# Kernel tuning notes

Measured on AMD Instinct MI355X. Metric: run time of the kernel, lower is better.

## Reference

```python
import math
import jax, jax.numpy as jnp
import numpy as np

B, W, C = 2, 2048, 1024
N, K = 16, 64  # heads, head dim (C // N)


def setup_inputs() -> dict:
    key = jax.random.key(0)
    ks = jax.random.split(key, 6)
    return {
        "in_sequence_bwc": jax.random.normal(ks[0], (B, W, C), dtype=jnp.float32),
        "W_proj": jax.random.normal(ks[1], (C, C), dtype=jnp.float32) * (1.0 / math.sqrt(C)),
        "b_proj": jax.random.normal(ks[2], (C,), dtype=jnp.float32) * 0.01,
        "generators_1nwk": jax.random.normal(ks[3], (1, N, W, K), dtype=jnp.float32),
        "W_mix": jax.random.normal(ks[4], (C, C), dtype=jnp.float32) * (1.0 / math.sqrt(C)),
        "b_mix": jax.random.normal(ks[5], (C,), dtype=jnp.float32) * 0.01,
    }


def reference(in_sequence_bwc, W_proj, b_proj, generators_1nwk, W_mix, b_mix):
    b, w, c = in_sequence_bwc.shape
    # shared projection (torch Linear: x @ W.T + b)
    p_bwc = in_sequence_bwc @ W_proj.T + b_proj
    p_bnwk = p_bwc.reshape(b, w, N, K).transpose(0, 2, 1, 3)  # [b, n, w, k]
    g_nwk = generators_1nwk[0, :, :w, :]  # [n, w, k]
    # data-dependent metric generator: p^T @ G -> [b, n, k, k]
    m_bnkk = jnp.einsum("bnwk,nwl->bnkl", p_bnwk, g_nwk)
    tril_kk = jnp.tril(jnp.ones((K, K), dtype=in_sequence_bwc.dtype))
    m_bnkk = m_bnkk * tril_kk  # lower-triangular mask on k x k
    m_bnkk = m_bnkk @ jnp.swapaxes(m_bnkk, -1, -2)  # PSD metric M M^T
    # bilinear scores: P @ M @ P^T, scaled
    pm_bnwk = jnp.einsum("bnwk,bnkl->bnwl", p_bnwk, m_bnkk)
    scores_bnww = jnp.einsum("bnwk,bnvk->bnwv", pm_bnwk, p_bnwk) / math.sqrt(K)
    causal = jnp.tril(jnp.ones((w, w), dtype=bool))
    scores_bnww = jnp.where(causal, scores_bnww, -jnp.inf)
    attn_bnww = jax.nn.softmax(scores_bnww, axis=-1)
    nudged_bnwk = attn_bnww @ p_bnwk
    nudged_bwc = nudged_bnwk.transpose(0, 2, 1, 3).reshape(b, w, c)
    return nudged_bwc @ W_mix.T + b_mix
```

## Files before the change

### kernel.cpp

```cpp
#include <hip/hip_runtime.h>
#include <math.h>

#define B_  2
#define W_  2048
#define C_  1024
#define NH_ 16
#define KD_ 64

__device__ __forceinline__ int sw(int r, int c) {
    return (r << 6) + ((((c >> 2) ^ ((r >> 2) & 7)) << 2) | (c & 3));
}

__device__ __forceinline__ void stage64s(const float* __restrict__ src,
                                         float* dst, int tid) {
#pragma unroll
    for (int q = 0; q < 4; ++q) {
        int idx = tid + (q << 8);
        int r   = idx >> 4;
        int c   = (idx & 15) << 2;
        *(float4*)&dst[sw(r, c)] = *(const float4*)(src + (idx << 2));
    }
}

__device__ __forceinline__ void stage64(const float* __restrict__ src,
                                        float (*dst)[68], int tid) {
#pragma unroll
    for (int q = 0; q < 4; ++q) {
        int idx = tid + (q << 8);
        int e   = idx << 2;
        int r   = e >> 6;
        int c   = e & 63;
        *(float4*)&dst[r][c] = *(const float4*)(src + e);
    }
}

template<int OUT_P_LAYOUT>
__global__ __launch_bounds__(256, 2)
void gemm_nt(const float* __restrict__ A, const float* __restrict__ Bw,
             const float* __restrict__ bias, float* __restrict__ Cout)
{
    __shared__ float As[16][68];
    __shared__ float Bs[16][68];
    const int tid = threadIdx.x;
    const int tx  = tid & 15, ty = tid >> 4;
    const int m0  = blockIdx.x << 6;
    const int n0  = blockIdx.y << 6;
    const int lrow = tid >> 2;
    const int lkq  = (tid & 3) << 2;
    const float* Ap = A  + (size_t)(m0 + lrow) * C_ + lkq;
    const float* Bp = Bw + (size_t)(n0 + lrow) * C_ + lkq;

    float acc[4][4] = {};
    for (int k0 = 0; k0 < C_; k0 += 16) {
        float4 av = *(const float4*)(Ap + k0);
        float4 bv = *(const float4*)(Bp + k0);
        __syncthreads();
        As[lkq+0][lrow] = av.x; As[lkq+1][lrow] = av.y;
        As[lkq+2][lrow] = av.z; As[lkq+3][lrow] = av.w;
        Bs[lkq+0][lrow] = bv.x; Bs[lkq+1][lrow] = bv.y;
        Bs[lkq+2][lrow] = bv.z; Bs[lkq+3][lrow] = bv.w;
        __syncthreads();
#pragma unroll
        for (int kk = 0; kk < 16; ++kk) {
            float4 a4 = *(const float4*)&As[kk][ty << 2];
            float4 b4 = *(const float4*)&Bs[kk][tx << 2];
            float am[4] = {a4.x, a4.y, a4.z, a4.w};
            float bm[4] = {b4.x, b4.y, b4.z, b4.w};
#pragma unroll
            for (int i = 0; i < 4; ++i)
#pragma unroll
                for (int j = 0; j < 4; ++j)
                    acc[i][j] = fmaf(am[i], bm[j], acc[i][j]);
        }
    }

    const int gc = n0 + (tx << 2);
    float4 bb = *(const float4*)&bias[gc];
#pragma unroll
    for (int i = 0; i < 4; ++i) {
        int gm = m0 + (ty << 2) + i;
        float4 o;
        o.x = acc[i][0] + bb.x;
        o.y = acc[i][1] + bb.y;
        o.z = acc[i][2] + bb.z;
        o.w = acc[i][3] + bb.w;
        if (OUT_P_LAYOUT) {
            int b = gm >> 11;
            int w = gm & 2047;
            int n = gc >> 6;
            int k = gc & 63;
            *(float4*)(Cout + (((size_t)(b * NH_ + n) * W_ + w) * KD_ + k)) = o;
        } else {
            *(float4*)(Cout + (size_t)gm * C_ + gc) = o;
        }
    }
}

__global__ __launch_bounds__(256, 2)
void metric_part(const float* __restrict__ p, const float* __restrict__ g,
                 float* __restrict__ part)
{
    __shared__ float Ps[32][68];
    __shared__ float Gs[32][68];
    const int ch  = blockIdx.x;
    const int bn  = blockIdx.y;
    const int n   = bn & (NH_ - 1);
    const int tid = threadIdx.x;
    const int tx  = tid & 15, ty = tid >> 4;
    const float* pb = p + (size_t)bn * W_ * KD_ + (size_t)(ch << 8) * KD_;
    const float* gb = g + (size_t)n  * W_ * KD_ + (size_t)(ch << 8) * KD_;

    float acc[4][4] = {};
    for (int w0 = 0; w0 < 256; w0 += 32) {
        __syncthreads();
#pragma unroll
        for (int q = 0; q < 2; ++q) {
            int idx = tid + (q << 8);
            int e   = idx << 2;
            int r   = e >> 6;
            int c   = e & 63;
            *(float4*)&Ps[r][c] = *(const float4*)(pb + (size_t)(w0 + r) * KD_ + c);
            *(float4*)&Gs[r][c] = *(const float4*)(gb + (size_t)(w0 + r) * KD_ + c);
        }
        __syncthreads();
#pragma unroll 8
        for (int w = 0; w < 32; ++w) {
            float4 a4 = *(const float4*)&Ps[w][ty << 2];
            float4 b4 = *(const float4*)&Gs[w][tx << 2];
            float am[4] = {a4.x, a4.y, a4.z, a4.w};
            float bm[4] = {b4.x, b4.y, b4.z, b4.w};
#pragma unroll
            for (int i = 0; i < 4; ++i)
#pragma unroll
                for (int j = 0; j < 4; ++j)
                    acc[i][j] = fmaf(am[i], bm[j], acc[i][j]);
        }
    }

    float* ob = part + (size_t)(bn * 8 + ch) * KD_ * KD_;
#pragma unroll
    for (int i = 0; i < 4; ++i) {
        float4 o; o.x = acc[i][0]; o.y = acc[i][1]; o.z = acc[i][2]; o.w = acc[i][3];
        *(float4*)(ob + ((ty << 2) + i) * KD_ + (tx << 2)) = o;
    }
}

__global__ __launch_bounds__(256, 2)
void metric_reduce(const float* __restrict__ part, float* __restrict__ m2)
{
    __shared__ float M1s[64][68];
    const int bn  = blockIdx.x;
    const int tid = threadIdx.x;
    const int tx  = tid & 15, ty = tid >> 4;
    const float* pb = part + (size_t)bn * 8 * KD_ * KD_;

#pragma unroll
    for (int v = 0; v < 4; ++v) {
        int f = tid + (v << 8);
        int e = f << 2;
        float4 s = *(const float4*)(pb + e);
#pragma unroll
        for (int c = 1; c < 8; ++c) {
            float4 t = *(const float4*)(pb + c * 4096 + e);
            s.x += t.x; s.y += t.y; s.z += t.z; s.w += t.w;
        }
        int k = e >> 6, l = e & 63;
        if (l + 0 > k) s.x = 0.f;
        if (l + 1 > k) s.y = 0.f;
        if (l + 2 > k) s.z = 0.f;
        if (l + 3 > k) s.w = 0.f;
        *(float4*)&M1s[k][l] = s;
    }
    __syncthreads();

    float a2[4][4] = {};
#pragma unroll
    for (int jq = 0; jq < 64; jq += 4) {
        float4 av[4], bv[4];
#pragma unroll
        for (int i = 0; i < 4; ++i) av[i] = *(const float4*)&M1s[(ty << 2) + i][jq];
#pragma unroll
        for (int j = 0; j < 4; ++j) bv[j] = *(const float4*)&M1s[(tx << 2) + j][jq];
#pragma unroll
        for (int i = 0; i < 4; ++i)
#pragma unroll
            for (int j = 0; j < 4; ++j)
                a2[i][j] += av[i].x * bv[j].x + av[i].y * bv[j].y +
                            av[i].z * bv[j].z + av[i].w * bv[j].w;
    }

    float* ob = m2 + (size_t)bn * KD_ * KD_;
#pragma unroll
    for (int i = 0; i < 4; ++i) {
        float4 o; o.x = a2[i][0]; o.y = a2[i][1]; o.z = a2[i][2]; o.w = a2[i][3];
        *(float4*)(ob + ((ty << 2) + i) * KD_ + (tx << 2)) = o;
    }
}

__global__ __launch_bounds__(256, 2)
void qgen_k(const float* __restrict__ p, const float* __restrict__ m2,
            float* __restrict__ qout)
{
    __shared__ float Pt[64][68];
    __shared__ float Ms[64][68];
    const int bn  = blockIdx.y;
    const int w0  = blockIdx.x << 6;
    const int tid = threadIdx.x;
    const int tx  = tid & 15, ty = tid >> 4;
    const float* pb = p  + (size_t)bn * W_ * KD_ + (size_t)w0 * KD_;
    const float* mb = m2 + (size_t)bn * KD_ * KD_;

    stage64(pb, Pt, tid);
    stage64(mb, Ms, tid);
    __syncthreads();

    float acc[4][4] = {};
#pragma unroll
    for (int kq = 0; kq < 64; kq += 4) {
        float4 av[4];
        float  bm[4][4];
#pragma unroll
        for (int i = 0; i < 4; ++i) av[i] = *(const float4*)&Pt[(ty << 2) + i][kq];
#pragma unroll
        for (int kk = 0; kk < 4; ++kk) {
            float4 t = *(const float4*)&Ms[kq + kk][tx << 2];
            bm[kk][0] = t.x; bm[kk][1] = t.y; bm[kk][2] = t.z; bm[kk][3] = t.w;
        }
#pragma unroll
        for (int i = 0; i < 4; ++i) {
            float am[4] = {av[i].x, av[i].y, av[i].z, av[i].w};
#pragma unroll
            for (int j = 0; j < 4; ++j)
                acc[i][j] = fmaf(am[0], bm[0][j],
                            fmaf(am[1], bm[1][j],
                            fmaf(am[2], bm[2][j],
                            fmaf(am[3], bm[3][j], acc[i][j]))));
        }
    }

    float* ob = qout + (size_t)bn * W_ * KD_ + (size_t)w0 * KD_;
#pragma unroll
    for (int i = 0; i < 4; ++i) {
        float4 o;
        o.x = acc[i][0] * 0.125f; o.y = acc[i][1] * 0.125f;
        o.z = acc[i][2] * 0.125f; o.w = acc[i][3] * 0.125f;
        *(float4*)(ob + ((ty << 2) + i) * KD_ + (tx << 2)) = o;
    }
}

__global__ __launch_bounds__(256, 2)
void attn_k(const float* __restrict__ qg, const float* __restrict__ p,
            float* __restrict__ nud)
{
    __shared__ float Qs[4096];
    __shared__ float Ks[2][4096];
    __shared__ float Es[4096];
    const int bid = blockIdx.x;
    const int bn  = bid & 31;
    const int qt  = (bid < 512) ? (31 - (bid >> 5)) : ((bid - 512) >> 5);
    const int b   = bn >> 4, n = bn & 15;
    const int tid = threadIdx.x;
    const int tx  = tid & 15, ty = tid >> 4;
    const float* qb = qg + (size_t)bn * W_ * KD_ + (size_t)(qt << 6) * KD_;
    const float* kb = p  + (size_t)bn * W_ * KD_;

    stage64s(qb, Qs, tid);
    stage64s(kb, Ks[0], tid);
    __syncthreads();

    float acc[4][4] = {};
    float mi[4], li[4];
#pragma unroll
    for (int i = 0; i < 4; ++i) { mi[i] = -INFINITY; li[i] = 0.f; }

    float4 ld[4];

    for (int j0 = 0; j0 <= qt; ++j0) {
        const int cur = j0 & 1;
        float* Kc = Ks[cur];

        if (j0 < qt) {
            const float* nx = kb + (size_t)((j0 + 1) << 6) * KD_;
#pragma unroll
            for (int q = 0; q < 4; ++q)
                ld[q] = *(const float4*)(nx + ((tid + (q << 8)) << 2));
        }

        float s[4][4] = {};
#pragma unroll
        for (int kq = 0; kq < 16; ++kq) {
            float4 av[4], bv[4];
#pragma unroll
            for (int i = 0; i < 4; ++i)
                av[i] = *(const float4*)&Qs[sw((ty << 2) + i, kq << 2)];
#pragma unroll
            for (int j = 0; j < 4; ++j)
                bv[j] = *(const float4*)&Kc[sw((tx << 2) + j, kq << 2)];
#pragma unroll
            for (int i = 0; i < 4; ++i)
#pragma unroll
                for (int j = 0; j < 4; ++j)
                    s[i][j] = fmaf(av[i].x, bv[j].x,
                              fmaf(av[i].y, bv[j].y,
                              fmaf(av[i].z, bv[j].z,
                              fmaf(av[i].w, bv[j].w, s[i][j]))));
        }

        if (j0 == qt) {
#pragma unroll
            for (int i = 0; i < 4; ++i)
#pragma unroll
                for (int j = 0; j < 4; ++j)
                    if (((tx << 2) + j) > ((ty << 2) + i)) s[i][j] = -INFINITY;
        }

        float mnew[4], al[4];
#pragma unroll
        for (int i = 0; i < 4; ++i) {
            float rm = fmaxf(fmaxf(s[i][0], s[i][1]), fmaxf(s[i][2], s[i][3]));
            rm = fmaxf(rm, __shfl_xor(rm, 1, 16));
            rm = fmaxf(rm, __shfl_xor(rm, 2, 16));
            rm = fmaxf(rm, __shfl_xor(rm, 4, 16));
            rm = fmaxf(rm, __shfl_xor(rm, 8, 16));
            mnew[i] = fmaxf(mi[i], rm);
        }
#pragma unroll
        for (int i = 0; i < 4; ++i) {
#pragma unroll
            for (int j = 0; j < 4; ++j) s[i][j] = __expf(s[i][j] - mnew[i]);
            float rs = s[i][0] + s[i][1] + s[i][2] + s[i][3];
            rs += __shfl_xor(rs, 1, 16);
            rs += __shfl_xor(rs, 2, 16);
            rs += __shfl_xor(rs, 4, 16);
            rs += __shfl_xor(rs, 8, 16);
            al[i] = __expf(mi[i] - mnew[i]);
            li[i] = li[i] * al[i] + rs;
            mi[i] = mnew[i];
        }

        __syncthreads();

#pragma unroll
        for (int i = 0; i < 4; ++i) {
            float4 e; e.x = s[i][0]; e.y = s[i][1]; e.z = s[i][2]; e.w = s[i][3];
            *(float4*)&Es[sw((ty << 2) + i, tx << 2)] = e;
#pragma unroll
            for (int j = 0; j < 4; ++j) acc[i][j] *= al[i];
        }
        if (j0 < qt) {
            float* Kn = Ks[cur ^ 1];
#pragma unroll
            for (int q = 0; q < 4; ++q) {
                int idx = tid + (q << 8);
                *(float4*)&Kn[sw(idx >> 4, (idx & 15) << 2)] = ld[q];
            }
        }
        __syncthreads();

#pragma unroll
        for (int jq = 0; jq < 64; jq += 4) {
            float4 av[4];
            float  vm[4][4];
#pragma unroll
            for (int i = 0; i < 4; ++i) av[i] = *(const float4*)&Es[sw((ty << 2) + i, jq)];
#pragma unroll
            for (int kk = 0; kk < 4; ++kk) {
                float4 t = *(const float4*)&Kc[sw(jq + kk, tx << 2)];
                vm[kk][0] = t.x; vm[kk][1] = t.y; vm[kk][2] = t.z; vm[kk][3] = t.w;
            }
#pragma unroll
            for (int i = 0; i < 4; ++i) {
                float am[4] = {av[i].x, av[i].y, av[i].z, av[i].w};
#pragma unroll
                for (int c = 0; c < 4; ++c)
                    acc[i][c] = fmaf(am[0], vm[0][c],
                                fmaf(am[1], vm[1][c],
                                fmaf(am[2], vm[2][c],
                                fmaf(am[3], vm[3][c], acc[i][c]))));
            }
        }
    }

    const int wrow = qt << 6;
#pragma unroll
    for (int i = 0; i < 4; ++i) {
        float inv = 1.f / li[i];
        float4 o;
        o.x = acc[i][0] * inv; o.y = acc[i][1] * inv;
        o.z = acc[i][2] * inv; o.w = acc[i][3] * inv;
        size_t row = (size_t)(b * W_ + wrow + (ty << 2) + i);
        *(float4*)(nud + row * C_ + (n << 6) + (tx << 2)) = o;
    }
}

extern "C" void kernel_launch(void* const* d_in, const int* in_sizes, int n_in,
                              void* d_out, int out_size, void* d_ws, size_t ws_size,
                              hipStream_t stream)
{
    (void)in_sizes; (void)n_in; (void)out_size; (void)ws_size;
    const float* X  = (const float*)d_in[0];
    const float* Wp = (const float*)d_in[1];
    const float* bp = (const float*)d_in[2];
    const float* G  = (const float*)d_in[3];
    const float* Wm = (const float*)d_in[4];
    const float* bm = (const float*)d_in[5];
    float* out = (float*)d_out;
    float* ws  = (float*)d_ws;

    float* Pbuf = ws;
    float* Qbuf = ws + 4194304;
    float* M2   = ws + 8388608;
    float* Nud  = ws + 8519680;
    float* Part = Qbuf;

    dim3 blk(256);
    gemm_nt<1>   <<<dim3(64, 16), blk, 0, stream>>>(X, Wp, bp, Pbuf);
    metric_part  <<<dim3(8, 32),  blk, 0, stream>>>(Pbuf, G, Part);
    metric_reduce<<<dim3(32),     blk, 0, stream>>>(Part, M2);
    qgen_k       <<<dim3(32, 32), blk, 0, stream>>>(Pbuf, M2, Qbuf);
    attn_k       <<<dim3(1024),   blk, 0, stream>>>(Qbuf, Pbuf, Nud);
    gemm_nt<0>   <<<dim3(64, 16), blk, 0, stream>>>(Nud, Wm, bm, out);
}
```

Baseline: 802.6 us.

## Software-pipeline attention loop: compute next QK^T while doing current PV

Restructures the flash-attention loop so that the scores and softmax for key tile p0+1 are computed in the same iteration as the P·V accumulation for tile p0. The probability tile is double-buffered and the loop keeps a single barrier per iteration instead of two. Q and V (the p tile) are now read straight from global memory through L1/L2 rather than from shared memory, which frees LDS but sends more traffic to the cache. K is prefetched two tiles ahead. The pipelining is meant to cut barrier stalls and overlap work, at the cost of more register pressure and global load latency.

```diff
diff --git a/kernel.cpp b/kernel.cpp
--- a/kernel.cpp
+++ b/kernel.cpp
@@ -252,9 +252,8 @@
 void attn_k(const float* __restrict__ qg, const float* __restrict__ p,
             float* __restrict__ nud)
 {
-    __shared__ float Qs[4096];
     __shared__ float Ks[2][4096];
-    __shared__ float Es[4096];
+    __shared__ float Es[2][4096];
     const int bid = blockIdx.x;
     const int bn  = bid & 31;
     const int qt  = (bid < 512) ? (31 - (bid >> 5)) : ((bid - 512) >> 5);
@@ -264,38 +263,35 @@
     const float* qb = qg + (size_t)bn * W_ * KD_ + (size_t)(qt << 6) * KD_;
     const float* kb = p  + (size_t)bn * W_ * KD_;
 
-    stage64s(qb, Qs, tid);
     stage64s(kb, Ks[0], tid);
+    float4 ld[4];
+    if (qt >= 1) {
+        const float* nx = kb + (size_t)KD_ * 64;
+#pragma unroll
+        for (int q = 0; q < 4; ++q)
+            ld[q] = *(const float4*)(nx + ((tid + (q << 8)) << 2));
+    }
     __syncthreads();
 
     float acc[4][4] = {};
-    float mi[4], li[4];
-#pragma unroll
-    for (int i = 0; i < 4; ++i) { mi[i] = -INFINITY; li[i] = 0.f; }
-
-    float4 ld[4];
-
-    for (int j0 = 0; j0 <= qt; ++j0) {
-        const int cur = j0 & 1;
-        float* Kc = Ks[cur];
-
-        if (j0 < qt) {
-            const float* nx = kb + (size_t)((j0 + 1) << 6) * KD_;
-#pragma unroll
-            for (int q = 0; q < 4; ++q)
-                ld[q] = *(const float4*)(nx + ((tid + (q << 8)) << 2));
-        }
-
+    float mi[4], li[4], al[4];
+#pragma unroll
+    for (int i = 0; i < 4; ++i) { mi[i] = -INFINITY; li[i] = 0.f; al[i] = 0.f; }
+
+    const float* qv = qb;
+
+    {
+        asm volatile("" : "+v"(qv));
         float s[4][4] = {};
 #pragma unroll
         for (int kq = 0; kq < 16; ++kq) {
             float4 av[4], bv[4];
 #pragma unroll
             for (int i = 0; i < 4; ++i)
-                av[i] = *(const float4*)&Qs[sw((ty << 2) + i, kq << 2)];
+                av[i] = *(const float4*)(qv + ((ty << 2) + i) * KD_ + (kq << 2));
 #pragma unroll
             for (int j = 0; j < 4; ++j)
-                bv[j] = *(const float4*)&Kc[sw((tx << 2) + j, kq << 2)];
+                bv[j] = *(const float4*)&Ks[0][sw((tx << 2) + j, kq << 2)];
 #pragma unroll
             for (int i = 0; i < 4; ++i)
 #pragma unroll
@@ -305,16 +301,13 @@
                               fmaf(av[i].z, bv[j].z,
                               fmaf(av[i].w, bv[j].w, s[i][j]))));
         }
-
-        if (j0 == qt) {
+        if (qt == 0) {
 #pragma unroll
             for (int i = 0; i < 4; ++i)
 #pragma unroll
                 for (int j = 0; j < 4; ++j)
                     if (((tx << 2) + j) > ((ty << 2) + i)) s[i][j] = -INFINITY;
         }
-
-        float mnew[4], al[4];
 #pragma unroll
         for (int i = 0; i < 4; ++i) {
             float rm = fmaxf(fmaxf(s[i][0], s[i][1]), fmaxf(s[i][2], s[i][3]));
@@ -322,33 +315,133 @@
             rm = fmaxf(rm, __shfl_xor(rm, 2, 16));
             rm = fmaxf(rm, __shfl_xor(rm, 4, 16));
             rm = fmaxf(rm, __shfl_xor(rm, 8, 16));
-            mnew[i] = fmaxf(mi[i], rm);
-        }
-#pragma unroll
-        for (int i = 0; i < 4; ++i) {
-#pragma unroll
-            for (int j = 0; j < 4; ++j) s[i][j] = __expf(s[i][j] - mnew[i]);
+            float mnew = fmaxf(mi[i], rm);
+#pragma unroll
+            for (int j = 0; j < 4; ++j) s[i][j] = __expf(s[i][j] - mnew);
             float rs = s[i][0] + s[i][1] + s[i][2] + s[i][3];
             rs += __shfl_xor(rs, 1, 16);
             rs += __shfl_xor(rs, 2, 16);
             rs += __shfl_xor(rs, 4, 16);
             rs += __shfl_xor(rs, 8, 16);
-            al[i] = __expf(mi[i] - mnew[i]);
+            al[i] = __expf(mi[i] - mnew);
             li[i] = li[i] * al[i] + rs;
-            mi[i] = mnew[i];
-        }
-
-        __syncthreads();
-
+            mi[i] = mnew;
+        }
 #pragma unroll
         for (int i = 0; i < 4; ++i) {
             float4 e; e.x = s[i][0]; e.y = s[i][1]; e.z = s[i][2]; e.w = s[i][3];
-            *(float4*)&Es[sw((ty << 2) + i, tx << 2)] = e;
+            *(float4*)&Es[0][sw((ty << 2) + i, tx << 2)] = e;
+        }
+        if (qt >= 1) {
+#pragma unroll
+            for (int q = 0; q < 4; ++q) {
+                int idx = tid + (q << 8);
+                *(float4*)&Ks[1][sw(idx >> 4, (idx & 15) << 2)] = ld[q];
+            }
+        }
+        __syncthreads();
+    }
+
+    for (int p0 = 0; p0 <= qt; ++p0) {
+        asm volatile("" : "+v"(qv));
+
+        if (p0 + 2 <= qt) {
+            const float* nx = kb + (size_t)((p0 + 2) << 6) * KD_;
+#pragma unroll
+            for (int q = 0; q < 4; ++q)
+                ld[q] = *(const float4*)(nx + ((tid + (q << 8)) << 2));
+        }
+
+#pragma unroll
+        for (int i = 0; i < 4; ++i)
 #pragma unroll
             for (int j = 0; j < 4; ++j) acc[i][j] *= al[i];
-        }
-        if (j0 < qt) {
-            float* Kn = Ks[cur ^ 1];
+
+        if (p0 < qt) {
+            const float* Kc = Ks[(p0 + 1) & 1];
+            float s[4][4] = {};
+#pragma unroll
+            for (int kq = 0; kq < 16; ++kq) {
+                float4 av[4], bv[4];
+#pragma unroll
+                for (int i = 0; i < 4; ++i)
+                    av[i] = *(const float4*)(qv + ((ty << 2) + i) * KD_ + (kq << 2));
+#pragma unroll
+                for (int j = 0; j < 4; ++j)
+                    bv[j] = *(const float4*)&Kc[sw((tx << 2) + j, kq << 2)];
+#pragma unroll
+                for (int i = 0; i < 4; ++i)
+#pragma unroll
+                    for (int j = 0; j < 4; ++j)
+                        s[i][j] = fmaf(av[i].x, bv[j].x,
+                                  fmaf(av[i].y, bv[j].y,
+                                  fmaf(av[i].z, bv[j].z,
+                                  fmaf(av[i].w, bv[j].w, s[i][j]))));
+            }
+            if (p0 + 1 == qt) {
+#pragma unroll
+                for (int i = 0; i < 4; ++i)
+#pragma unroll
+                    for (int j = 0; j < 4; ++j)
+                        if (((tx << 2) + j) > ((ty << 2) + i)) s[i][j] = -INFINITY;
+            }
+#pragma unroll
+            for (int i = 0; i < 4; ++i) {
+                float rm = fmaxf(fmaxf(s[i][0], s[i][1]), fmaxf(s[i][2], s[i][3]));
+                rm = fmaxf(rm, __shfl_xor(rm, 1, 16));
+                rm = fmaxf(rm, __shfl_xor(rm, 2, 16));
+                rm = fmaxf(rm, __shfl_xor(rm, 4, 16));
+                rm = fmaxf(rm, __shfl_xor(rm, 8, 16));
+                float mnew = fmaxf(mi[i], rm);
+#pragma unroll
+                for (int j = 0; j < 4; ++j) s[i][j] = __expf(s[i][j] - mnew);
+                float rs = s[i][0] + s[i][1] + s[i][2] + s[i][3];
+                rs += __shfl_xor(rs, 1, 16);
+                rs += __shfl_xor(rs, 2, 16);
+                rs += __shfl_xor(rs, 4, 16);
+                rs += __shfl_xor(rs, 8, 16);
+                al[i] = __expf(mi[i] - mnew);
+                li[i] = li[i] * al[i] + rs;
+                mi[i] = mnew;
+            }
+            float* Ew = Es[(p0 + 1) & 1];
+#pragma unroll
+            for (int i = 0; i < 4; ++i) {
+                float4 e; e.x = s[i][0]; e.y = s[i][1]; e.z = s[i][2]; e.w = s[i][3];
+                *(float4*)&Ew[sw((ty << 2) + i, tx << 2)] = e;
+            }
+        }
+
+        {
+            const float* kt = kb + (size_t)(p0 << 6) * KD_;
+            const float* Ec = Es[p0 & 1];
+#pragma unroll
+            for (int jq = 0; jq < 64; jq += 4) {
+                float4 av[4];
+                float  vm[4][4];
+#pragma unroll
+                for (int i = 0; i < 4; ++i)
+                    av[i] = *(const float4*)&Ec[sw((ty << 2) + i, jq)];
+#pragma unroll
+                for (int kk = 0; kk < 4; ++kk) {
+                    float4 t = *(const float4*)(kt + (size_t)(jq + kk) * KD_ + (tx << 2));
+                    vm[kk][0] = t.x; vm[kk][1] = t.y; vm[kk][2] = t.z; vm[kk][3] = t.w;
+                }
+#pragma unroll
+                for (int i = 0; i < 4; ++i) {
+                    float am[4] = {av[i].x, av[i].y, av[i].z, av[i].w};
+#pragma unroll
+                    for (int c = 0; c < 4; ++c)
+                        acc[i][c] = fmaf(am[0], vm[0][c],
+                                    fmaf(am[1], vm[1][c],
+                                    fmaf(am[2], vm[2][c],
+                                    fmaf(am[3], vm[3][c], acc[i][c]))));
+                }
+            }
+        }
+
+        if (p0 + 2 <= qt) {
+            float* Kn = Ks[p0 & 1];
 #pragma unroll
             for (int q = 0; q < 4; ++q) {
                 int idx = tid + (q << 8);
@@ -356,29 +449,6 @@
             }
         }
         __syncthreads();
-
-#pragma unroll
-        for (int jq = 0; jq < 64; jq += 4) {
-            float4 av[4];
-            float  vm[4][4];
-#pragma unroll
-            for (int i = 0; i < 4; ++i) av[i] = *(const float4*)&Es[sw((ty << 2) + i, jq)];
-#pragma unroll
-            for (int kk = 0; kk < 4; ++kk) {
-                float4 t = *(const float4*)&Kc[sw(jq + kk, tx << 2)];
-                vm[kk][0] = t.x; vm[kk][1] = t.y; vm[kk][2] = t.z; vm[kk][3] = t.w;
-            }
-#pragma unroll
-            for (int i = 0; i < 4; ++i) {
-                float am[4] = {av[i].x, av[i].y, av[i].z, av[i].w};
-#pragma unroll
-                for (int c = 0; c < 4; ++c)
-                    acc[i][c] = fmaf(am[0], vm[0][c],
-                                fmaf(am[1], vm[1][c],
-                                fmaf(am[2], vm[2][c],
-                                fmaf(am[3], vm[3][c], acc[i][c]))));
-            }
-        }
     }
 
     const int wrow = qt << 6;
```

Measured after the change: 2.462 ms. 3.07x slower.
